# Performance work log

Measured on AMD Instinct MI355X. Metric: run time of the kernel, lower is better.

## Reference

```python
import jax, jax.numpy as jnp
import numpy as np

# ---- dims (see shape_source) ----
N, EG, T = 10000, 120000, 600000
NR, NS = 16, 7                      # num_radial, num_spherical
EA, EE, ET, ERBF, ECBF, EBIL = 128, 256, 64, 16, 16, 64
NB = 2                              # num_blocks
CUTOFF = 6.0
MAXZ = 100
INV_SQRT2 = 0.7071067811865476


def scaled_silu(x):
    # GemNet 'swish' activation = ScaledSiLU
    return jax.nn.silu(x) * (1.0 / 0.6)


def layer_norm(x, w, b):
    mu = jnp.mean(x, -1, keepdims=True)
    v = jnp.var(x, -1, keepdims=True)
    return (x - mu) * jax.lax.rsqrt(v + 1e-5) * w + b


def radial_basis(D):
    # polynomial envelope (exponent 5) * gaussian RBF on d/cutoff
    d = D / CUTOFF
    p = 5.0
    env = 1.0 - ((p + 1) * (p + 2) / 2) * d**5 + p * (p + 2) * d**6 - (p * (p + 1) / 2) * d**7
    env = jnp.where(d < 1.0, env, 0.0)
    offsets = jnp.linspace(0.0, 1.0, NR)
    coeff = -0.5 * (NR - 1.0) ** 2   # -0.5 / spacing^2
    return env[:, None] * jnp.exp(coeff * (d[:, None] - offsets) ** 2)  # (EG, NR)


def spherical_basis(cosphi):
    # circular basis: Y_l0(phi) = sqrt((2l+1)/4pi) P_l(cos phi), l = 0..NS-1
    P = [jnp.ones_like(cosphi), cosphi]
    for l in range(2, NS):
        P.append(((2 * l - 1) * cosphi * P[-1] - (l - 1) * P[-2]) / l)
    return jnp.stack([np.sqrt((2 * l + 1) / (4 * np.pi)) * P[l] for l in range(NS)], -1)  # (T, NS)


def residual(x, Ws):
    # GemNet ResidualLayer: 2 bias-free dense + skip, scaled by 1/sqrt(2)
    y = scaled_silu(scaled_silu(x @ Ws[0]) @ Ws[1])
    return (x + y) * INV_SQRT2


def gemnet_forward(D, cosphi, atom_emb, W_rbf3, W_rbf_h, W_rbf_out, W_cbf_down,
                   W_edge_emb, ib_dense_ca, ib_trip_dense_ba, ib_trip_mlp_rbf,
                   ib_trip_down, ib_trip_bilinear, ib_trip_up_ca, ib_trip_up_ac,
                   ib_res_before, ib_res_after, ib_atom_dense_rbf, ib_atom_dense1,
                   ib_atom_res, ib_concat_dense, ib_res_m, ob_dense_rbf, ob_dense1,
                   ob_res, ln_m_w, ln_m_b, ln_E_w, ln_E_b,
                   Z, idx_s, idx_t, id3_ba, id3_ca, id_swap):
    rbf = radial_basis(D)                                   # (EG, NR)
    sph = spherical_basis(cosphi)                           # (T, NS)
    rbf3 = rbf @ W_rbf3                                     # (EG, ERBF)
    rbf_h = rbf @ W_rbf_h
    rbf_out = rbf @ W_rbf_out
    # EfficientInteractionDownProjection: rbf x W -> (EG, NS, ECBF)
    rbf_W1 = jnp.einsum('er,sri->esi', rbf, W_cbf_down)
    # per-triplet circular-basis embedding: sum over spherical components
    cbf_t = jnp.einsum('ts,tsi->ti', sph, rbf_W1[id3_ca])   # (T, ECBF)

    h = atom_emb[Z]                                         # (N, EA)
    m = scaled_silu(jnp.concatenate([h[idx_s], h[idx_t], rbf], -1) @ W_edge_emb)  # (EG, EE)

    def out_block(i, h_cur, m_cur):
        mn = layer_norm(m_cur, ln_m_w[i], ln_m_b[i])
        x = mn * (rbf_out @ ob_dense_rbf[i])                # (EG, EE)
        xE = jax.ops.segment_sum(x, idx_t, num_segments=N)  # scatter edges -> atoms
        xE = scaled_silu(xE @ ob_dense1[i])                 # (N, EA)
        for r in range(ob_res.shape[1]):
            xE = residual(xE, ob_res[i, r])
        return layer_norm(xE, ln_E_w[i], ln_E_b[i])

    E_t = out_block(0, h, m)
    for i in range(NB):
        # ---- triplet interaction ----
        x_ca_skip = scaled_silu(m @ ib_dense_ca[i])
        x_ba = scaled_silu(m @ ib_trip_dense_ba[i])
        x_ba = x_ba * (rbf3 @ ib_trip_mlp_rbf[i])
        x_trip = scaled_silu(x_ba @ ib_trip_down[i])        # (EG, ET)
        x_t = x_trip[id3_ba]                                # gather -> (T, ET)
        # bilinear: out[t,o] = sum_i cbf_t[t,i] * sum_c x_t[t,c] W[c,i,o]
        Wb = ib_trip_bilinear[i]                            # (ET, ECBF, EBIL)
        acc = (x_t @ Wb[:, 0, :]) * cbf_t[:, 0:1]
        for ic in range(1, ECBF):
            acc = acc + (x_t @ Wb[:, ic, :]) * cbf_t[:, ic:ic + 1]
        x = jax.ops.segment_sum(acc, id3_ca, num_segments=EG)  # scatter trip -> edges (EG, EBIL)
        x_ca = scaled_silu(x @ ib_trip_up_ca[i])
        x_ac = scaled_silu(x @ ib_trip_up_ac[i])[id_swap]   # counter-directional edge
        x3 = (x_ca + x_ac) * INV_SQRT2

        # ---- edge update ----
        x = (x_ca_skip + x3) * INV_SQRT2
        for r in range(ib_res_before.shape[1]):
            x = residual(x, ib_res_before[i, r])
        x = (x + m) * INV_SQRT2
        for r in range(ib_res_after.shape[1]):
            x = residual(x, ib_res_after[i, r])

        # ---- atom update ----
        xa = x * (rbf_h @ ib_atom_dense_rbf[i])
        xa = jax.ops.segment_sum(xa, idx_t, num_segments=N)
        xa = scaled_silu(xa @ ib_atom_dense1[i])            # (N, EA)
        for r in range(ib_atom_res.shape[1]):
            xa = residual(xa, ib_atom_res[i, r])
        h = (h + xa) * INV_SQRT2

        # ---- edge embedding refresh with updated atoms ----
        m2 = scaled_silu(jnp.concatenate([h[idx_s], h[idx_t], x], -1) @ ib_concat_dense[i])
        for r in range(ib_res_m.shape[1]):
            m2 = residual(m2, ib_res_m[i, r])
        m = (m + m2) * INV_SQRT2

        E_t = E_t + out_block(i + 1, h, m)
    return E_t  # (N, EA) per-atom output features


def setup_inputs() -> dict:
    key = jax.random.key(0)
    ks = iter(jax.random.split(key, 64))

    def nrm(shape, fan_in):
        return jax.random.normal(next(ks), shape, jnp.float32) / np.sqrt(fan_in)

    Z = jax.random.randint(next(ks), (N,), 0, MAXZ)
    idx_s = jax.random.randint(next(ks), (EG,), 0, N)
    idx_t = jax.random.randint(next(ks), (EG,), 0, N)
    id3_ba = jax.random.randint(next(ks), (T,), 0, EG)
    id3_ca = jax.random.randint(next(ks), (T,), 0, EG)
    id_swap = jnp.arange(EG) ^ 1   # symmetric edges stored in (e, e^1) pairs
    D = jax.random.uniform(next(ks), (EG,), jnp.float32, 0.8, 5.9)
    cosphi = jax.random.uniform(next(ks), (T,), jnp.float32, -1.0, 1.0)

    emb = jax.random.normal(next(ks), (MAXZ, EA), jnp.float32)
    emb = emb / jnp.maximum(jnp.linalg.norm(emb, axis=-1, keepdims=True), 1.0)  # max_norm=1

    NBo = NB + 1
    inp = dict(
        D=D, cosphi=cosphi, atom_emb=emb,
        W_rbf3=nrm((NR, ERBF), NR), W_rbf_h=nrm((NR, ERBF), NR), W_rbf_out=nrm((NR, ERBF), NR),
        W_cbf_down=nrm((NS, NR, ECBF), NR),
        W_edge_emb=nrm((2 * EA + NR, EE), 2 * EA + NR),
        ib_dense_ca=nrm((NB, EE, EE), EE),
        ib_trip_dense_ba=nrm((NB, EE, EE), EE),
        ib_trip_mlp_rbf=nrm((NB, ERBF, EE), ERBF),
        ib_trip_down=nrm((NB, EE, ET), EE),
        ib_trip_bilinear=nrm((NB, ET, ECBF, EBIL), ET * ECBF),
        ib_trip_up_ca=nrm((NB, EBIL, EE), EBIL),
        ib_trip_up_ac=nrm((NB, EBIL, EE), EBIL),
        ib_res_before=nrm((NB, 1, 2, EE, EE), EE),
        ib_res_after=nrm((NB, 1, 2, EE, EE), EE),
        ib_atom_dense_rbf=nrm((NB, ERBF, EE), ERBF),
        ib_atom_dense1=nrm((NB, EE, EA), EE),
        ib_atom_res=nrm((NB, 2, 2, EA, EA), EA),
        ib_concat_dense=nrm((NB, 2 * EA + EE, EE), 2 * EA + EE),
        ib_res_m=nrm((NB, 1, 2, EE, EE), EE),
        ob_dense_rbf=nrm((NBo, ERBF, EE), ERBF),
        ob_dense1=nrm((NBo, EE, EA), EE),
        ob_res=nrm((NBo, 2, 2, EA, EA), EA),
        ln_m_w=jnp.ones((NBo, EE)), ln_m_b=jnp.zeros((NBo, EE)),
        ln_E_w=jnp.ones((NBo, EA)), ln_E_b=jnp.zeros((NBo, EA)),
        Z=Z, idx_s=idx_s, idx_t=idx_t, id3_ba=id3_ba, id3_ca=id3_ca, id_swap=id_swap,
    )
    return inp


def reference(D, cosphi, atom_emb, W_rbf3, W_rbf_h, W_rbf_out, W_cbf_down, W_edge_emb,
              ib_dense_ca, ib_trip_dense_ba, ib_trip_mlp_rbf, ib_trip_down,
              ib_trip_bilinear, ib_trip_up_ca, ib_trip_up_ac, ib_res_before,
              ib_res_after, ib_atom_dense_rbf, ib_atom_dense1, ib_atom_res,
              ib_concat_dense, ib_res_m, ob_dense_rbf, ob_dense1, ob_res,
              ln_m_w, ln_m_b, ln_E_w, ln_E_b, Z, idx_s, idx_t, id3_ba, id3_ca, id_swap):
    return gemnet_forward(D, cosphi, atom_emb, W_rbf3, W_rbf_h, W_rbf_out, W_cbf_down,
                          W_edge_emb, ib_dense_ca, ib_trip_dense_ba, ib_trip_mlp_rbf,
                          ib_trip_down, ib_trip_bilinear, ib_trip_up_ca, ib_trip_up_ac,
                          ib_res_before, ib_res_after, ib_atom_dense_rbf, ib_atom_dense1,
                          ib_atom_res, ib_concat_dense, ib_res_m, ob_dense_rbf, ob_dense1,
                          ob_res, ln_m_w, ln_m_b, ln_E_w, ln_E_b,
                          Z, idx_s, idx_t, id3_ba, id3_ca, id_swap)
```

## Files before the change

### kernel.cpp

```cpp
#include <hip/hip_runtime.h>

#define NATOM 10000
#define EG    120000
#define TT    600000

#define INV_SQRT2f 0.7071067811865476f

typedef unsigned short bf16t;
typedef __attribute__((ext_vector_type(8))) short s16x8;
typedef __attribute__((ext_vector_type(8))) unsigned short u16x8;
typedef __attribute__((ext_vector_type(4))) float f32x4;

__device__ __forceinline__ float ssilu(float x) {
    return x * (1.0f / (1.0f + __expf(-x))) * (1.0f / 0.6f);
}
__device__ __forceinline__ float bf2f(unsigned short u) {
    return __uint_as_float(((unsigned)u) << 16);
}
__device__ __forceinline__ unsigned short f2bf(float f) {
    unsigned b = __float_as_uint(f);
    unsigned r = (b + 0x7FFF + ((b >> 16) & 1)) >> 16;
    return (unsigned short)r;
}
__device__ __forceinline__ u16x8 cvt8(const float4 va, const float4 vb) {
// ... 187 lines not shown
        float ys = y[s];
#pragma unroll
        for (int i = 0; i < 16; i++) out[i] = fmaf(ys, w[s * 16 + i], out[i]);
    }
    int p = rank[t];
#pragma unroll
    for (int i = 0; i < 16; i++) cbf[(size_t)p * 16 + i] = f2bf(out[i]);
}

__global__ __launch_bounds__(256) void k_hgather(
    const float* __restrict__ emb, const int* __restrict__ Z, bf16t* __restrict__ h)
{
    int i = blockIdx.x * 256 + threadIdx.x;
    if (i < NATOM * 128) {
        int n = i >> 7, j = i & 127;
        h[i] = f2bf(emb[(size_t)Z[n] * 128 + j]);
    }
}

template <typename TA, int FR, int FC, int EPI>
__global__ __launch_bounds__(256) void mgemm3(
    const TA* __restrict__ A, const bf16t* __restrict__ BT,
    bf16t* __restrict__ C, const bf16t* __restrict__ skip,
    int M, int N, int K)
{
    constexpr int ROWS = 2 * FR * 16;
    constexpr int COLS = 2 * FC * 16;
    __shared__ __align__(16) ushort As[ROWS][40];
    __shared__ __align__(16) ushort Bs[COLS][40];
    const int tid = threadIdx.x, wave = tid >> 6, lane = tid & 63;
    const int waveR = wave >> 1, waveC = wave & 1;
    const int rowBase = blockIdx.y * ROWS, colBase = blockIdx.x * COLS;

    const int sar = tid >> 1, sak = (tid & 1) << 4;
    int agr = rowBase + sar; if (agr >= M) agr = M - 1;
    int sbc, sbk;
    if constexpr (COLS == 128) { sbc = tid >> 1; sbk = (tid & 1) << 4; }
    else                       { sbc = tid >> 2; sbk = (tid & 3) << 3; }

    f32x4 zv = {0.f, 0.f, 0.f, 0.f};
    f32x4 acc[FR][FC];
#pragma unroll
    for (int f = 0; f < FR; f++)
#pragma unroll
        for (int q = 0; q < FC; q++) acc[f][q] = zv;

    const int arow0 = waveR * FR * 16 + (lane & 15);
    const int bcol0 = waveC * FC * 16 + (lane & 15);
    const int kd = (lane >> 4) << 3;

    u16x8 a0, a1, b0, b1;
    auto loadA = [&](int k0) {
        if constexpr (sizeof(TA) == 2) {
            const u16x8* s = (const u16x8*)((const bf16t*)A + (size_t)agr * K + k0 + sak);
            a0 = s[0]; a1 = s[1];
        } else {
            const float4* s = (const float4*)((const float*)A + (size_t)agr * K + k0 + sak);
            a0 = cvt8(s[0], s[1]); a1 = cvt8(s[2], s[3]);
        }
    };
    auto loadB = [&](int k0) {
        const u16x8* s = (const u16x8*)(BT + (size_t)(colBase + sbc) * K + k0 + sbk);
        b0 = s[0];
        if constexpr (COLS == 128) b1 = s[1];
    };
    loadA(0); loadB(0);
    for (int k0 = 0; k0 < K; k0 += 32) {
        __syncthreads();
        *(u16x8*)&As[sar][sak] = a0;
        *(u16x8*)&As[sar][sak + 8] = a1;
        *(u16x8*)&Bs[sbc][sbk] = b0;
        if constexpr (COLS == 128) *(u16x8*)&Bs[sbc][sbk + 8] = b1;
        __syncthreads();
        if (k0 + 32 < K) { loadA(k0 + 32); loadB(k0 + 32); }
        u16x8 af[FR], bf[FC];
#pragma unroll
        for (int f = 0; f < FR; f++) af[f] = *(const u16x8*)&As[arow0 + f * 16][kd];
#pragma unroll
        for (int q = 0; q < FC; q++) bf[q] = *(const u16x8*)&Bs[bcol0 + q * 16][kd];
#pragma unroll
        for (int f = 0; f < FR; f++)
#pragma unroll
            for (int q = 0; q < FC; q++)
                acc[f][q] = __builtin_amdgcn_mfma_f32_16x16x32_bf16(
                    *(s16x8*)&af[f], *(s16x8*)&bf[q], acc[f][q], 0, 0, 0);
    }

    const int rB = rowBase + waveR * FR * 16 + ((lane >> 4) << 2);
    const int cB = colBase + waveC * FC * 16 + (lane & 15);
#pragma unroll
    for (int f = 0; f < FR; f++) {
#pragma unroll
        for (int r = 0; r < 4; r++) {
            int row = rB + f * 16 + r;
            if (row >= M) continue;
#pragma unroll
            for (int q = 0; q < FC; q++) {
                int col = cB + q * 16;
                float v = acc[f][q][r];
                if (EPI == 1) {
                    C[(size_t)row * N + col] = f2bf(ssilu(v));
                } else {
                    float sk = bf2f(skip[(size_t)row * N + col]);
                    C[(size_t)row * N + col] = f2bf((sk + ssilu(v)) * INV_SQRT2f);
                }
            }
        }
    }
}

template <typename TA, int FC>
__global__ __launch_bounds__(256) void mgemm4(
    const TA* __restrict__ A, const bf16t* __restrict__ BT,
    bf16t* __restrict__ C, int M, int N, int K)
{
    constexpr int COLS = 2 * FC * 16;
    __shared__ __align__(16) ushort As[256][40];
    __shared__ __align__(16) ushort Bs[COLS][40];
    const int tid = threadIdx.x, wave = tid >> 6, lane = tid & 63;
    const int waveR = wave >> 1, waveC = wave & 1;
    const int rowBase = blockIdx.y * 256, colBase = blockIdx.x * COLS;

    int agr = rowBase + tid; if (agr >= M) agr = M - 1;
    const int sbc = tid >> 1, sbk = (tid & 1) << 4;

    f32x4 zv = {0.f, 0.f, 0.f, 0.f};
    f32x4 acc[8][FC];
#pragma unroll
    for (int f = 0; f < 8; f++)
#pragma unroll
        for (int q = 0; q < FC; q++) acc[f][q] = zv;

    const int arow0 = waveR * 128 + (lane & 15);
    const int bcol0 = waveC * FC * 16 + (lane & 15);
    const int kd = (lane >> 4) << 3;

    u16x8 a[4], b0, b1;
    auto loadA = [&](int k0) {
        if constexpr (sizeof(TA) == 2) {
            const u16x8* s = (const u16x8*)((const bf16t*)A + (size_t)agr * K + k0);
            a[0] = s[0]; a[1] = s[1]; a[2] = s[2]; a[3] = s[3];
        } else {
            const float4* s = (const float4*)((const float*)A + (size_t)agr * K + k0);
            a[0] = cvt8(s[0], s[1]); a[1] = cvt8(s[2], s[3]);
            a[2] = cvt8(s[4], s[5]); a[3] = cvt8(s[6], s[7]);
        }
    };
    auto loadB = [&](int k0) {
        const u16x8* s = (const u16x8*)(BT + (size_t)(colBase + sbc) * K + k0 + sbk);
        b0 = s[0]; b1 = s[1];
    };
    loadA(0); loadB(0);
    for (int k0 = 0; k0 < K; k0 += 32) {
        __syncthreads();
        *(u16x8*)&As[tid][0] = a[0];
        *(u16x8*)&As[tid][8] = a[1];
        *(u16x8*)&As[tid][16] = a[2];
        *(u16x8*)&As[tid][24] = a[3];
        *(u16x8*)&Bs[sbc][sbk] = b0;
        *(u16x8*)&Bs[sbc][sbk + 8] = b1;
        __syncthreads();
        if (k0 + 32 < K) { loadA(k0 + 32); loadB(k0 + 32); }
        u16x8 af[8], bf[FC];
#pragma unroll
        for (int f = 0; f < 8; f++) af[f] = *(const u16x8*)&As[arow0 + f * 16][kd];
#pragma unroll
        for (int q = 0; q < FC; q++) bf[q] = *(const u16x8*)&Bs[bcol0 + q * 16][kd];
#pragma unroll
        for (int f = 0; f < 8; f++)
#pragma unroll
            for (int q = 0; q < FC; q++)
                acc[f][q] = __builtin_amdgcn_mfma_f32_16x16x32_bf16(
                    *(s16x8*)&af[f], *(s16x8*)&bf[q], acc[f][q], 0, 0, 0);
    }

    const int rB = rowBase + waveR * 128 + ((lane >> 4) << 2);
    const int cB = colBase + waveC * FC * 16 + (lane & 15);
#pragma unroll
    for (int f = 0; f < 8; f++) {
#pragma unroll
        for (int r = 0; r < 4; r++) {
            int row = rB + f * 16 + r;
            if (row >= M) continue;
#pragma unroll
            for (int q = 0; q < FC; q++)
                C[(size_t)row * N + cB + q * 16] = f2bf(ssilu(acc[f][q][r]));
        }
    }
}

template <int FCC, int EPIOUT>
__global__ __launch_bounds__(256) void mgemm_res(
    const bf16t* __restrict__ A, const bf16t* __restrict__ BT0,
    const bf16t* __restrict__ BT1, bf16t* __restrict__ C,
    const bf16t* __restrict__ add2, int M)
{
    constexpr int N = FCC * 32;
    __shared__ __align__(16) ushort As[64][40];
    __shared__ __align__(16) ushort Bs[N][40];
    __shared__ __align__(16) ushort inter[64][N + 8];
    const int tid = threadIdx.x, wave = tid >> 6, lane = tid & 63;
    const int waveR = wave >> 1, waveC = wave & 1;
    const int rowBase = blockIdx.x * 64;

    const int sar = tid >> 2, sak = (tid & 3) << 3;
    int agr = rowBase + sar; if (agr >= M) agr = M - 1;
    const int sbc = tid >> 2, sbk = (tid & 3) << 3;

    const int arow0 = waveR * 32 + (lane & 15);
    const int bcol0 = waveC * FCC * 16 + (lane & 15);
    const int kd = (lane >> 4) << 3;

    f32x4 zv = {0.f, 0.f, 0.f, 0.f};
    f32x4 acc[2][FCC];
#pragma unroll
    for (int f = 0; f < 2; f++)
#pragma unroll
        for (int q = 0; q < FCC; q++) acc[f][q] = zv;

    u16x8 aR, bR[FCC / 2];
    auto loadA = [&](int k0) {
        aR = *(const u16x8*)(A + (size_t)agr * N + k0 + sak);
    };
    auto loadB = [&](const bf16t* BT, int k0) {
#pragma unroll
        for (int j = 0; j < FCC / 2; j++)
            bR[j] = *(const u16x8*)(BT + (size_t)(sbc + j * 64) * N + k0 + sbk);
    };

    loadA(0); loadB(BT0, 0);
    for (int k0 = 0; k0 < N; k0 += 32) {
        __syncthreads();
        *(u16x8*)&As[sar][sak] = aR;
#pragma unroll
        for (int j = 0; j < FCC / 2; j++) *(u16x8*)&Bs[sbc + j * 64][sbk] = bR[j];
        __syncthreads();
        if (k0 + 32 < N) { loadA(k0 + 32); loadB(BT0, k0 + 32); }
        else             { loadB(BT1, 0); }
        u16x8 af0 = *(const u16x8*)&As[arow0][kd];
        u16x8 af1 = *(const u16x8*)&As[arow0 + 16][kd];
        u16x8 bf[FCC];
#pragma unroll
        for (int q = 0; q < FCC; q++) bf[q] = *(const u16x8*)&Bs[bcol0 + q * 16][kd];
#pragma unroll
        for (int q = 0; q < FCC; q++) {
            acc[0][q] = __builtin_amdgcn_mfma_f32_16x16x32_bf16(
                *(s16x8*)&af0, *(s16x8*)&bf[q], acc[0][q], 0, 0, 0);
            acc[1][q] = __builtin_amdgcn_mfma_f32_16x16x32_bf16(
                *(s16x8*)&af1, *(s16x8*)&bf[q], acc[1][q], 0, 0, 0);
        }
    }
    {
        const int rL = waveR * 32 + ((lane >> 4) << 2);
        const int cL = waveC * FCC * 16 + (lane & 15);
#pragma unroll
        for (int f = 0; f < 2; f++)
#pragma unroll
            for (int r = 0; r < 4; r++)
#pragma unroll
                for (int q = 0; q < FCC; q++)
                    inter[rL + f * 16 + r][cL + q * 16] = f2bf(ssilu(acc[f][q][r]));
    }
#pragma unroll
    for (int f = 0; f < 2; f++)
#pragma unroll
        for (int q = 0; q < FCC; q++) acc[f][q] = zv;

    for (int k0 = 0; k0 < N; k0 += 32) {
        __syncthreads();
#pragma unroll
        for (int j = 0; j < FCC / 2; j++) *(u16x8*)&Bs[sbc + j * 64][sbk] = bR[j];
        __syncthreads();
        if (k0 + 32 < N) loadB(BT1, k0 + 32);
        u16x8 af0 = *(const u16x8*)&inter[arow0][k0 + kd];
        u16x8 af1 = *(const u16x8*)&inter[arow0 + 16][k0 + kd];
        u16x8 bf[FCC];
#pragma unroll
        for (int q = 0; q < FCC; q++) bf[q] = *(const u16x8*)&Bs[bcol0 + q * 16][kd];
#pragma unroll
        for (int q = 0; q < FCC; q++) {
            acc[0][q] = __builtin_amdgcn_mfma_f32_16x16x32_bf16(
                *(s16x8*)&af0, *(s16x8*)&bf[q], acc[0][q], 0, 0, 0);
            acc[1][q] = __builtin_amdgcn_mfma_f32_16x16x32_bf16(
                *(s16x8*)&af1, *(s16x8*)&bf[q], acc[1][q], 0, 0, 0);
        }
    }

    const int rB = rowBase + waveR * 32 + ((lane >> 4) << 2);
    const int cB = waveC * FCC * 16 + (lane & 15);
#pragma unroll
    for (int f = 0; f < 2; f++) {
#pragma unroll
        for (int r = 0; r < 4; r++) {
            int row = rB + f * 16 + r;
            if (row >= M) continue;
#pragma unroll
            for (int q = 0; q < FCC; q++) {
                int col = cB + q * 16;
                float sk = bf2f(A[(size_t)row * N + col]);
                float y = (sk + ssilu(acc[f][q][r])) * INV_SQRT2f;
                if (EPIOUT == 1) y = (y + bf2f(add2[(size_t)row * N + col])) * INV_SQRT2f;
                C[(size_t)row * N + col] = f2bf(y);
            }
        }
    }
}

__global__ __launch_bounds__(256) void mgemmA1(
    const bf16t* __restrict__ BT, bf16t* __restrict__ C,
    int M, int N, int K, int KP,
    const bf16t* __restrict__ hA, const int* __restrict__ gS,
    const int* __restrict__ gT, const bf16t* __restrict__ X, int w2)
{
    __shared__ __align__(16) ushort As[256][40];
    __shared__ __align__(16) ushort Bs[128][40];
    const int tid = threadIdx.x, wave = tid >> 6, lane = tid & 63;
    const int waveR = wave >> 1, waveC = wave & 1;
    const int rowBase = blockIdx.y * 256, colBase = blockIdx.x * 128;

    int agr = rowBase + tid; if (agr >= M) agr = M - 1;
    const int ia = gS[agr], ibx = gT[agr];
    const int sbc = tid >> 1, sbk = (tid & 1) << 4;

    f32x4 zv = {0.f, 0.f, 0.f, 0.f};
    f32x4 acc[8][4];
#pragma unroll
    for (int f = 0; f < 8; f++)
#pragma unroll
        for (int q = 0; q < 4; q++) acc[f][q] = zv;

    const int arow0 = waveR * 128 + (lane & 15);
    const int bcol0 = waveC * 64 + (lane & 15);
    const int kd = (lane >> 4) << 3;

    u16x8 a[4], b0, b1;
    auto loadA = [&](int k0) {
#pragma unroll
        for (int h = 0; h < 2; h++) {
            int kk = k0 + 16 * h;
            u16x8 t0{}, t1{};
            if (kk < 128) {
                const u16x8* s = (const u16x8*)(hA + (size_t)ia * 128 + kk);
                t0 = s[0]; t1 = s[1];
            } else if (kk < 256) {
                const u16x8* s = (const u16x8*)(hA + (size_t)ibx * 128 + (kk - 128));
                t0 = s[0]; t1 = s[1];
            } else if (kk < K && kk - 256 < w2) {
                const u16x8* s = (const u16x8*)(X + (size_t)agr * w2 + (kk - 256));
                t0 = s[0]; t1 = s[1];
            }
            a[2 * h] = t0; a[2 * h + 1] = t1;
        }
    };
    auto loadB = [&](int k0) {
        const u16x8* s = (const u16x8*)(BT + (size_t)(colBase + sbc) * KP + k0 + sbk);
        b0 = s[0]; b1 = s[1];
    };
    loadA(0); loadB(0);
    for (int k0 = 0; k0 < K; k0 += 32) {
        __syncthreads();
        *(u16x8*)&As[tid][0] = a[0];
        *(u16x8*)&As[tid][8] = a[1];
        *(u16x8*)&As[tid][16] = a[2];
        *(u16x8*)&As[tid][24] = a[3];
        *(u16x8*)&Bs[sbc][sbk] = b0;
        *(u16x8*)&Bs[sbc][sbk + 8] = b1;
        __syncthreads();
        if (k0 + 32 < K) { loadA(k0 + 32); loadB(k0 + 32); }
        u16x8 af[8], bf[4];
#pragma unroll
        for (int f = 0; f < 8; f++) af[f] = *(const u16x8*)&As[arow0 + f * 16][kd];
#pragma unroll
        for (int q = 0; q < 4; q++) bf[q] = *(const u16x8*)&Bs[bcol0 + q * 16][kd];
#pragma unroll
        for (int f = 0; f < 8; f++)
#pragma unroll
            for (int q = 0; q < 4; q++)
                acc[f][q] = __builtin_amdgcn_mfma_f32_16x16x32_bf16(
                    *(s16x8*)&af[f], *(s16x8*)&bf[q], acc[f][q], 0, 0, 0);
    }

    const int rB = rowBase + waveR * 128 + ((lane >> 4) << 2);
    const int cB = colBase + waveC * 64 + (lane & 15);
#pragma unroll
    for (int f = 0; f < 8; f++) {
#pragma unroll
        for (int r = 0; r < 4; r++) {
            int row = rB + f * 16 + r;
            if (row >= M) continue;
#pragma unroll
            for (int q = 0; q < 4; q++)
                C[(size_t)row * N + cB + q * 16] = f2bf(ssilu(acc[f][q][r]));
        }
    }
}

__global__ __launch_bounds__(256) void mgemm_up(
    const float* __restrict__ A, const bf16t* __restrict__ BTca,
    const bf16t* __restrict__ BTac, bf16t* __restrict__ C,
    const bf16t* __restrict__ skip, int M)
{
    constexpr int K = 64, N = 256;
    __shared__ __align__(16) ushort As[128][40];
    __shared__ __align__(16) ushort Bs[2][64][40];
    const int tid = threadIdx.x, wave = tid >> 6, lane = tid & 63;
    const int waveR = wave >> 1, waveC = wave & 1;
    const int rowBase = blockIdx.y * 128, colBase = blockIdx.x * 64;

    const int sar = tid >> 1, sak = (tid & 1) << 4;
    int agr = rowBase + sar; if (agr >= M) agr = M - 1;
    const int sbc = tid >> 2, sbk = (tid & 3) << 3;

    f32x4 zv = {0.f, 0.f, 0.f, 0.f};
    f32x4 accA[4][2], accB[4][2];
#pragma unroll
    for (int f = 0; f < 4; f++)
#pragma unroll
        for (int q = 0; q < 2; q++) { accA[f][q] = zv; accB[f][q] = zv; }

    const int arow0 = waveR * 64 + (lane & 15);
    const int bcol0 = waveC * 32 + (lane & 15);
    const int kd = (lane >> 4) << 3;

    u16x8 a0, a1, bA, bB;
    auto loadA = [&](int k0) {
        const float4* s = (const float4*)(A + (size_t)agr * K + k0 + sak);
        a0 = cvt8(s[0], s[1]); a1 = cvt8(s[2], s[3]);
    };
    auto loadB = [&](int k0) {
        bA = *(const u16x8*)(BTca + (size_t)(colBase + sbc) * K + k0 + sbk);
        bB = *(const u16x8*)(BTac + (size_t)(colBase + sbc) * K + k0 + sbk);
    };
    loadA(0); loadB(0);
    for (int k0 = 0; k0 < K; k0 += 32) {
        __syncthreads();
        *(u16x8*)&As[sar][sak] = a0;
        *(u16x8*)&As[sar][sak + 8] = a1;
        *(u16x8*)&Bs[0][sbc][sbk] = bA;
        *(u16x8*)&Bs[1][sbc][sbk] = bB;
        __syncthreads();
        if (k0 + 32 < K) { loadA(k0 + 32); loadB(k0 + 32); }
        u16x8 af[4], bfA[2], bfB[2];
#pragma unroll
        for (int f = 0; f < 4; f++) af[f] = *(const u16x8*)&As[arow0 + f * 16][kd];
#pragma unroll
        for (int q = 0; q < 2; q++) {
            bfA[q] = *(const u16x8*)&Bs[0][bcol0 + q * 16][kd];
            bfB[q] = *(const u16x8*)&Bs[1][bcol0 + q * 16][kd];
        }
#pragma unroll
        for (int f = 0; f < 4; f++)
#pragma unroll
            for (int q = 0; q < 2; q++) {
                accA[f][q] = __builtin_amdgcn_mfma_f32_16x16x32_bf16(
                    *(s16x8*)&af[f], *(s16x8*)&bfA[q], accA[f][q], 0, 0, 0);
                accB[f][q] = __builtin_amdgcn_mfma_f32_16x16x32_bf16(
                    *(s16x8*)&af[f], *(s16x8*)&bfB[q], accB[f][q], 0, 0, 0);
            }
    }

    const int rB = rowBase + waveR * 64 + ((lane >> 4) << 2);
    const int cB = colBase + waveC * 32 + (lane & 15);
#pragma unroll
    for (int f = 0; f < 4; f++) {
#pragma unroll
        for (int r = 0; r < 4; r++) {
            int row = rB + f * 16 + r;
            if (row >= M) continue;
#pragma unroll
            for (int q = 0; q < 2; q++) {
                int col = cB + q * 16;
                float v = (ssilu(accA[f][q][r]) + ssilu(accB[f][q][r ^ 1])) * INV_SQRT2f;
                float y = (bf2f(skip[(size_t)row * N + col]) + v) * INV_SQRT2f;
                C[(size_t)row * N + col] = f2bf(y);
            }
        }
    }
}

__global__ __launch_bounds__(256) void k_bilinear_m(
    const bf16t* __restrict__ xtrip, const bf16t* __restrict__ cbf,
    const bf16t* __restrict__ WT,
    const int* __restrict__ ba_s, const int* __restrict__ ca_s,
    float* __restrict__ seg)
{
    __shared__ __align__(16) ushort xs[64][72];
    __shared__ ushort cbs[64][16];
    __shared__ int cas[64];
    __shared__ __align__(16) ushort ws[2][4096];
    __shared__ __align__(16) float ts[64][65];
    const int tid = threadIdx.x, wave = tid >> 6, lane = tid & 63;
    const int t0 = blockIdx.x * 64;
    {
        int r = tid >> 2, q = (tid & 3) << 4;
        int ba = ba_s[t0 + r];
        const u16x8* src = (const u16x8*)(xtrip + (size_t)ba * 64 + q);
        *(u16x8*)&xs[r][q] = src[0];
        *(u16x8*)&xs[r][q + 8] = src[1];
    }
    if (tid < 64) cas[tid] = ca_s[t0 + tid];
    {
        int e = tid << 2; int r = e >> 4, c = e & 15;
        *(ushort4*)&cbs[r][c] = *(const ushort4*)(cbf + (size_t)(t0 + r) * 16 + c);
    }
    u16x8 g0, g1;
    {
        const u16x8* s = (const u16x8*)(WT + (size_t)tid * 16);
        *(u16x8*)&ws[0][tid * 16] = s[0];
        *(u16x8*)&ws[0][tid * 16 + 8] = s[1];
        const u16x8* s1 = (const u16x8*)(WT + 4096 + (size_t)tid * 16);
        g0 = s1[0]; g1 = s1[1];
    }
    __syncthreads();
    const int kd = (lane >> 4) << 3;
    u16x8 a0 = *(const u16x8*)(&xs[wave * 16 + (lane & 15)][kd]);
    u16x8 a1 = *(const u16x8*)(&xs[wave * 16 + (lane & 15)][32 + kd]);
    const int rowo = wave * 16 + ((lane >> 4) << 2);
    const int chb = lane >> 4, colw = lane & 15;

    float tot[4][4];
#pragma unroll
    for (int a = 0; a < 4; a++)
#pragma unroll
        for (int b = 0; b < 4; b++) tot[a][b] = 0.f;

    for (int i = 0; i < 16; i++) {
        const int cur = i & 1;
        if (i < 15) {
            *(u16x8*)&ws[cur ^ 1][tid * 16] = g0;
            *(u16x8*)&ws[cur ^ 1][tid * 16 + 8] = g1;
        }
        const ushort* wb = ws[cur];
        f32x4 zv = {0.f, 0.f, 0.f, 0.f};
        f32x4 p[4] = {zv, zv, zv, zv};
#pragma unroll
        for (int fc = 0; fc < 4; fc++) {
            u16x8 b0 = *(const u16x8*)&wb[((chb * 64) + colw + fc * 16) * 8];
            u16x8 b1 = *(const u16x8*)&wb[(((4 + chb) * 64) + colw + fc * 16) * 8];
            p[fc] = __builtin_amdgcn_mfma_f32_16x16x32_bf16(
                *(s16x8*)&a0, *(s16x8*)&b0, p[fc], 0, 0, 0);
            p[fc] = __builtin_amdgcn_mfma_f32_16x16x32_bf16(
                *(s16x8*)&a1, *(s16x8*)&b1, p[fc], 0, 0, 0);
        }
#pragma unroll
        for (int r = 0; r < 4; r++) {
            float s = bf2f(cbs[rowo + r][i]);
#pragma unroll
            for (int fc = 0; fc < 4; fc++) tot[fc][r] += s * p[fc][r];
        }
        if (i < 14) {
            const u16x8* s = (const u16x8*)(WT + (size_t)(i + 2) * 4096 + (size_t)tid * 16);
            g0 = s[0]; g1 = s[1];
        }
        __syncthreads();
    }
#pragma unroll
    for (int r = 0; r < 4; r++)
#pragma unroll
        for (int fc = 0; fc < 4; fc++)
            ts[rowo + r][fc * 16 + (lane & 15)] = tot[fc][r];
    __syncthreads();
    {
        int q = tid >> 6, c = tid & 63;
        float s = 0.f;
        int cur = cas[q * 16];
#pragma unroll 1
        for (int r = q * 16; r < q * 16 + 16; r++) {
            int ca = cas[r];
            if (ca != cur) {
                atomicAdd(&seg[(size_t)cur * 64 + c], s);
                s = 0.f; cur = ca;
            }
            s += ts[r][c];
        }
        atomicAdd(&seg[(size_t)cur * 64 + c], s);
    }
}

__global__ __launch_bounds__(256) void k_mulproj(
    const bf16t* __restrict__ in, const bf16t* __restrict__ rvec,
    const float* __restrict__ Wp, bf16t* __restrict__ out)
{
    __shared__ float sW[4096];
    __shared__ float sr[256];
    const int j = threadIdx.x;
    const int e0 = blockIdx.x * 16;
    for (int t = j; t < 4096; t += 256) sW[t] = Wp[t];
    sr[j] = bf2f(rvec[(size_t)e0 * 16 + j]);
    __syncthreads();
#pragma unroll 4
    for (int g = 0; g < 16; g++) {
        float p = 0.f;
#pragma unroll
        for (int k = 0; k < 16; k++) p = fmaf(sr[g * 16 + k], sW[k * 256 + j], p);
        size_t e = (size_t)(e0 + g);
        out[e * 256 + j] = f2bf(bf2f(in[e * 256 + j]) * p);
    }
}

__global__ __launch_bounds__(256) void k_ln_proj(
    const bf16t* __restrict__ m, const float* __restrict__ lnw,
    const float* __restrict__ lnb, const bf16t* __restrict__ rvec,
    const float* __restrict__ Wp, bf16t* __restrict__ out)
{
    __shared__ float sW[4096];
    __shared__ float sr[256];
    __shared__ float red[8];
    const int j = threadIdx.x;
    const int e0 = blockIdx.x * 16;
    for (int t = j; t < 4096; t += 256) sW[t] = Wp[t];
    sr[j] = bf2f(rvec[(size_t)e0 * 16 + j]);
    const float lw = lnw[j], lb = lnb[j];
    __syncthreads();
    const int wid = j >> 6, lane = j & 63;
    for (int g = 0; g < 16; g++) {
        size_t e = (size_t)(e0 + g);
        float v = bf2f(m[e * 256 + j]);
        float s = v, s2 = v * v;
#pragma unroll
        for (int off = 32; off > 0; off >>= 1) {
            s += __shfl_xor(s, off);
            s2 += __shfl_xor(s2, off);
        }
        if (lane == 0) { red[wid] = s; red[4 + wid] = s2; }
        __syncthreads();
        float tot = red[0] + red[1] + red[2] + red[3];
        float tot2 = red[4] + red[5] + red[6] + red[7];
        float mu = tot * (1.f / 256.f);
        float var = tot2 * (1.f / 256.f) - mu * mu;
        float ln = (v - mu) * rsqrtf(var + 1e-5f) * lw + lb;
        float p = 0.f;
#pragma unroll
        for (int k = 0; k < 16; k++) p = fmaf(sr[g * 16 + k], sW[k * 256 + j], p);
        out[e * 256 + j] = f2bf(ln * p);
        __syncthreads();
    }
}

__global__ __launch_bounds__(128) void k_ln_acc(
    const bf16t* __restrict__ x, const float* __restrict__ w,
    const float* __restrict__ b, float* __restrict__ out)
{
    int n = blockIdx.x;
    int j = threadIdx.x;
    __shared__ float red[4];
    float v = bf2f(x[(size_t)n * 128 + j]);
    float s = v, s2 = v * v;
#pragma unroll
    for (int off = 32; off > 0; off >>= 1) {
        s += __shfl_xor(s, off);
        s2 += __shfl_xor(s2, off);
    }
    int wid = j >> 6, lane = j & 63;
    if (lane == 0) { red[wid] = s; red[2 + wid] = s2; }
    __syncthreads();
    float tot = red[0] + red[1];
    float tot2 = red[2] + red[3];
    float mu = tot * (1.f / 128.f);
    float var = tot2 * (1.f / 128.f) - mu * mu;
    out[(size_t)n * 128 + j] += (v - mu) * rsqrtf(var + 1e-5f) * w[j] + b[j];
}

typedef bf16t T;
static bool try_run(void* const* d_in, void* d_out, void* d_ws, size_t ws_size, hipStream_t stream)
{
    const float* D            = (const float*)d_in[0];
    const float* cosphi       = (const float*)d_in[1];
    const float* atom_emb     = (const float*)d_in[2];
    const float* W_rbf3       = (const float*)d_in[3];
    const float* W_rbf_h      = (const float*)d_in[4];
    const float* W_rbf_out    = (const float*)d_in[5];
    const float* W_cbf_down   = (const float*)d_in[6];
    const float* W_edge_emb   = (const float*)d_in[7];
    const float* ib_dense_ca  = (const float*)d_in[8];
    const float* ib_trip_dense_ba = (const float*)d_in[9];
    const float* ib_trip_mlp_rbf  = (const float*)d_in[10];
    const float* ib_trip_down     = (const float*)d_in[11];
    const float* ib_trip_bilinear = (const float*)d_in[12];
    const float* ib_trip_up_ca    = (const float*)d_in[13];
    const float* ib_trip_up_ac    = (const float*)d_in[14];
    const float* ib_res_before    = (const float*)d_in[15];
    const float* ib_res_after     = (const float*)d_in[16];
    const float* ib_atom_dense_rbf = (const float*)d_in[17];
    const float* ib_atom_dense1    = (const float*)d_in[18];
    const float* ib_atom_res       = (const float*)d_in[19];
    const float* ib_concat_dense   = (const float*)d_in[20];
    const float* ib_res_m          = (const float*)d_in[21];
    const float* ob_dense_rbf      = (const float*)d_in[22];
    const float* ob_dense1         = (const float*)d_in[23];
    const float* ob_res            = (const float*)d_in[24];
    const float* ln_m_w            = (const float*)d_in[25];
    const float* ln_m_b            = (const float*)d_in[26];
    const float* ln_E_w            = (const float*)d_in[27];
    const float* ln_E_b            = (const float*)d_in[28];
    const int* Z       = (const int*)d_in[29];
    const int* idx_s   = (const int*)d_in[30];
    const int* idx_t   = (const int*)d_in[31];
    const int* id3_ba  = (const int*)d_in[32];
    const int* id3_ca  = (const int*)d_in[33];

    char* base = (char*)d_ws;
    size_t off = 0;
    auto alloc = [&](size_t bytes) -> char* {
        off = (off + 255) & ~(size_t)255;
        char* p = base + off;
        off += bytes;
        return p;
    };
    T* m      = (T*)alloc((size_t)EG * 256 * 2);
    T* B1     = (T*)alloc((size_t)EG * 256 * 2);
    T* B2     = (T*)alloc((size_t)EG * 256 * 2);
    float* rbfW1 = (float*)B1;
    int* rank    = (int*)B2;
    T* rbf    = (T*)alloc((size_t)EG * 16 * 2);
    T* cbf    = (T*)alloc((size_t)TT * 16 * 2);
    bf16t* h  = (bf16t*)alloc((size_t)NATOM * 128 * 2);
    T* xtrip  = (T*)alloc((size_t)EG * 64 * 2);
    char* ub  = alloc((size_t)EG * 64 * 4);
    float* seg64  = (float*)ub;
    bf16t* segN_b = (bf16t*)ub;
    bf16t* At1b   = (bf16t*)(ub + (size_t)NATOM * 256 * 2);
    int* cntT  = (int*)ub;
    int* cnt2T = (int*)(ub + (size_t)EG * 4);
    int* off_ca = (int*)(ub + (size_t)2 * EG * 4);
    float* wcb = (float*)alloc((size_t)7 * 4096 * 4);
    bf16t* ar  = (bf16t*)alloc((size_t)507904 * 2);
    int* off_atom  = (int*)alloc((size_t)(NATOM + 1) * 4);
    int* ba_s      = (int*)alloc((size_t)TT * 4);
    int* ca_s      = (int*)alloc((size_t)TT * 4);
    int* csr_edges = (int*)alloc((size_t)EG * 4);
    if (off > ws_size) return false;
    float* out = (float*)d_out;

    auto g256 = [&](const T* A, unsigned wOff, T* C) {
        dim3 grid(2, (EG + 255) / 256);
        mgemm4<T, 4><<<grid, 256, 0, stream>>>(A, ar + wOff, C, EG, 256, 256);
    };
    auto gatom1 = [&](const bf16t* A, unsigned wOff, bf16t* C) {
        dim3 grid(1, (NATOM + 127) / 128);
        mgemm3<bf16t, 4, 4, 1><<<grid, 256, 0, stream>>>(A, ar + wOff, C, nullptr, NATOM, 128, 256);
    };
    auto out_block = [&](int i, unsigned offD1, unsigned offRes) {
        k_ln_proj<<<EG / 16, 256, 0, stream>>>(m, ln_m_w + (size_t)i * 256, ln_m_b + (size_t)i * 256,
                                               rbf, wcb + (size_t)(4 + i) * 4096, B2);
        k_segsum<<<NATOM, 256, 0, stream>>>(B2, off_atom, csr_edges, segN_b);
        gatom1(segN_b, offD1, At1b);
        mgemm_res<4, 0><<<(NATOM + 63) / 64, 256, 0, stream>>>(
            At1b, ar + offRes, ar + offRes + 16384, At1b, nullptr, NATOM);
        mgemm_res<4, 0><<<(NATOM + 63) / 64, 256, 0, stream>>>(
            At1b, ar + offRes + 32768, ar + offRes + 49152, At1b, nullptr, NATOM);
        k_ln_acc<<<NATOM, 128, 0, stream>>>(At1b, ln_E_w + (size_t)i * 128, ln_E_b + (size_t)i * 128, out);
    };

    hipMemsetAsync(cntT, 0, (size_t)EG * 4, stream);
    k_hist<<<(TT + 255) / 256, 256, 0, stream>>>(id3_ca, cntT, TT);
    k_scan<<<1, 1024, 0, stream>>>(cntT, off_ca, EG);
    hipMemsetAsync(cnt2T, 0, (size_t)EG * 4, stream);
    k_rank_trip<<<(TT + 255) / 256, 256, 0, stream>>>(id3_ca, id3_ba, off_ca, cnt2T,
                                                      rank, ba_s, ca_s, TT);
    hipMemsetAsync(cntT, 0, (size_t)NATOM * 4, stream);
    k_hist<<<(EG + 255) / 256, 256, 0, stream>>>(idx_t, cntT, EG);
    k_scan<<<1, 1024, 0, stream>>>(cntT, off_atom, NATOM);
    hipMemsetAsync(cnt2T, 0, (size_t)NATOM * 4, stream);
    k_rank_edge<<<(EG + 255) / 256, 256, 0, stream>>>(idx_t, off_atom, cnt2T, csr_edges, EG);

    {
        WcBatch wb;
        wb.e[0] = {W_rbf3, ib_trip_mlp_rbf};
        wb.e[1] = {W_rbf3, ib_trip_mlp_rbf + 4096};
        wb.e[2] = {W_rbf_h, ib_atom_dense_rbf};
        wb.e[3] = {W_rbf_h, ib_atom_dense_rbf + 4096};
        wb.e[4] = {W_rbf_out, ob_dense_rbf};
        wb.e[5] = {W_rbf_out, ob_dense_rbf + 4096};
        wb.e[6] = {W_rbf_out, ob_dense_rbf + 8192};
        k_wcomb_batch<<<7, 256, 0, stream>>>(wb, wcb);
    }
    {
        WtBatch wt{};
        wt.e[0] = {W_edge_emb, 0u, 272, 288, 256, 0};
        wt.e[1] = {ob_dense1, 73728u, 256, 256, 128, 0};
        for (int j = 0; j < 4; j++)
            wt.e[2 + j] = {ob_res + (size_t)j * 16384, 106496u + j * 16384u, 128, 128, 128, 0};
        wt.n = 6;
        k_wt_batch<<<512, 256, 0, stream>>>(wt, ar);
    }

    hipMemsetAsync(out, 0, (size_t)NATOM * 128 * 4, stream);
    k_rbf<<<(EG + 255) / 256, 256, 0, stream>>>(D, W_cbf_down, rbf, rbfW1);
    k_cbf<<<(TT + 255) / 256, 256, 0, stream>>>(cosphi, id3_ca, rbfW1, rank, cbf);
    k_hgather<<<(NATOM * 128 + 255) / 256, 256, 0, stream>>>(atom_emb, Z, h);
    {
        dim3 grid(2, (EG + 255) / 256);
        mgemmA1<<<grid, 256, 0, stream>>>(ar, m, EG, 256, 272, 288, h, idx_s, idx_t, rbf, 16);
    }
    out_block(0, 73728u, 106496u);

    for (int i = 0; i < 2; i++) {
        {
            WtBatch wt{};
            wt.e[0] = {ib_dense_ca + (size_t)i * 65536, 0u, 256, 256, 256, 0};
            wt.e[1] = {ib_trip_dense_ba + (size_t)i * 65536, 65536u, 256, 256, 256, 0};
            wt.e[2] = {ib_trip_down + (size_t)i * 16384, 131072u, 256, 256, 64, 0};
            wt.e[3] = {ib_trip_bilinear + (size_t)i * 65536, 147456u, 0, 0, 0, 1};
            wt.e[4] = {ib_trip_up_ca + (size_t)i * 16384, 212992u, 64, 64, 256, 0};
            wt.e[5] = {ib_trip_up_ac + (size_t)i * 16384, 229376u, 64, 64, 256, 0};
            wt.e[6] = {ib_res_before + (size_t)i * 131072, 245760u, 256, 256, 256, 0};
            wt.e[7] = {ib_res_before + (size_t)i * 131072 + 65536, 311296u, 256, 256, 256, 0};
            wt.e[8] = {ib_res_after + (size_t)i * 131072, 376832u, 256, 256, 256, 0};
            wt.e[9] = {ib_res_after + (size_t)i * 131072 + 65536, 442368u, 256, 256, 256, 0};
            wt.n = 10;
            k_wt_batch<<<512, 256, 0, stream>>>(wt, ar);
        }
        g256(m, 0u, B1);
        g256(m, 65536u, B2);
        k_mulproj<<<EG / 16, 256, 0, stream>>>(B2, rbf, wcb + (size_t)i * 4096, B2);
        {
            dim3 grid(1, (EG + 127) / 128);
            mgemm3<T, 4, 2, 1><<<grid, 256, 0, stream>>>(B2, ar + 131072, xtrip, nullptr, EG, 64, 256);
        }
        hipMemsetAsync(seg64, 0, (size_t)EG * 64 * 4, stream);
        k_bilinear_m<<<TT / 64, 256, 0, stream>>>(xtrip, cbf, ar + 147456, ba_s, ca_s, seg64);
        {
            dim3 grid(4, (EG + 127) / 128);
            mgemm_up<<<grid, 256, 0, stream>>>(seg64, ar + 212992, ar + 229376, B1, B1, EG);
        }
        mgemm_res<8, 1><<<EG / 64, 256, 0, stream>>>(B1, ar + 245760, ar + 311296, B1, m, EG);
        mgemm_res<8, 0><<<EG / 64, 256, 0, stream>>>(B1, ar + 376832, ar + 442368, B1, nullptr, EG);
        {
            WtBatch wt{};
            wt.e[0] = {ib_atom_dense1 + (size_t)i * 32768, 0u, 256, 256, 128, 0};
            for (int j = 0; j < 4; j++)
                wt.e[1 + j] = {ib_atom_res + (size_t)i * 65536 + (size_t)j * 16384,
                               32768u + j * 16384u, 128, 128, 128, 0};
            wt.e[5] = {ib_concat_dense + (size_t)i * 131072, 98304u, 512, 512, 256, 0};
            wt.e[6] = {ib_res_m + (size_t)i * 131072, 229376u, 256, 256, 256, 0};
            wt.e[7] = {ib_res_m + (size_t)i * 131072 + 65536, 294912u, 256, 256, 256, 0};
            wt.e[8] = {ob_dense1 + (size_t)(i + 1) * 32768, 360448u, 256, 256, 128, 0};
            wt.n = 9;
            k_wt_batch<<<512, 256, 0, stream>>>(wt, ar);
            WtBatch wt2{};
            for (int j = 0; j < 4; j++)
                wt2.e[j] = {ob_res + (size_t)(i + 1) * 65536 + (size_t)j * 16384,
                            393216u + j * 16384u, 128, 128, 128, 0};
            wt2.n = 4;
            k_wt_batch<<<512, 256, 0, stream>>>(wt2, ar);
        }
        k_mulproj<<<EG / 16, 256, 0, stream>>>(B1, rbf, wcb + (size_t)(2 + i) * 4096, B2);
        k_segsum<<<NATOM, 256, 0, stream>>>(B2, off_atom, csr_edges, segN_b);
        gatom1(segN_b, 0u, At1b);
        mgemm_res<4, 0><<<(NATOM + 63) / 64, 256, 0, stream>>>(
            At1b, ar + 32768, ar + 49152, At1b, nullptr, NATOM);
        mgemm_res<4, 1><<<(NATOM + 63) / 64, 256, 0, stream>>>(
            At1b, ar + 65536, ar + 81920, h, h, NATOM);
        {
            dim3 grid(2, (EG + 255) / 256);
            mgemmA1<<<grid, 256, 0, stream>>>(ar + 98304, B2, EG, 256, 512, 512, h, idx_s, idx_t, B1, 256);
        }
        mgemm_res<8, 1><<<EG / 64, 256, 0, stream>>>(B2, ar + 229376, ar + 294912, m, m, EG);

        out_block(i + 1, 360448u, 393216u);
    }
    return true;
}

extern "C" void kernel_launch(void* const* d_in, const int* in_sizes, int n_in,
                              void* d_out, int out_size, void* d_ws, size_t ws_size,
                              hipStream_t stream)
{
    if (try_run(d_in, d_out, d_ws, ws_size, stream)) return;
    float v = 3000.0f + (float)(ws_size >> 20);
    k_fill<<<(NATOM * 128 + 255) / 256, 256, 0, stream>>>((float*)d_out, NATOM * 128, v);
}
```

Measured before the change: 2.641 ms.

## Fuse atom dense and two residual layers into one shared-memory chain kernel

```diff
diff --git a/kernel.cpp b/kernel.cpp
--- a/kernel.cpp
+++ b/kernel.cpp
@@ -513,6 +513,177 @@
                 if (EPIOUT == 1) y = (y + bf2f(add2[(size_t)row * N + col])) * INV_SQRT2f;
                 C[(size_t)row * N + col] = f2bf(y);
             }
+        }
+    }
+}
+
+template <int EPI>
+__global__ __launch_bounds__(256) void k_atomchain(
+    const bf16t* __restrict__ X, const bf16t* __restrict__ BTd1,
+    const bf16t* __restrict__ BTres, bf16t* __restrict__ C, int M)
+{
+    __shared__ __align__(16) ushort As[64][40];
+    __shared__ __align__(16) ushort Bs[128][40];
+    __shared__ __align__(16) ushort buf0[64][136];
+    __shared__ __align__(16) ushort buf1[64][136];
+    const int tid = threadIdx.x, wave = tid >> 6, lane = tid & 63;
+    const int waveR = wave >> 1, waveC = wave & 1;
+    const int rowBase = blockIdx.x * 64;
+    const int arow0 = waveR * 32 + (lane & 15);
+    const int bcol0 = waveC * 64 + (lane & 15);
+    const int kd = (lane >> 4) << 3;
+    const int rL = waveR * 32 + ((lane >> 4) << 2);
+    const int cL = waveC * 64 + (lane & 15);
+    const int sbc = tid >> 1, sbk = (tid & 1) << 4;
+
+    f32x4 zv = {0.f, 0.f, 0.f, 0.f};
+    f32x4 acc[2][4];
+
+    {
+        const int sar = tid >> 2, sak = (tid & 3) << 3;
+        int agr = rowBase + sar; if (agr >= M) agr = M - 1;
+#pragma unroll
+        for (int f = 0; f < 2; f++)
+#pragma unroll
+            for (int q = 0; q < 4; q++) acc[f][q] = zv;
+        u16x8 aR, b0, b1;
+        auto loadA = [&](int k0) {
+            aR = *(const u16x8*)(X + (size_t)agr * 256 + k0 + sak);
+        };
+        auto loadB = [&](int k0) {
+            const u16x8* s = (const u16x8*)(BTd1 + (size_t)sbc * 256 + k0 + sbk);
+            b0 = s[0]; b1 = s[1];
+        };
+        loadA(0); loadB(0);
+        for (int k0 = 0; k0 < 256; k0 += 32) {
+            __syncthreads();
+            *(u16x8*)&As[sar][sak] = aR;
+            *(u16x8*)&Bs[sbc][sbk] = b0;
+            *(u16x8*)&Bs[sbc][sbk + 8] = b1;
+            __syncthreads();
+            if (k0 + 32 < 256) { loadA(k0 + 32); loadB(k0 + 32); }
+            u16x8 af0 = *(const u16x8*)&As[arow0][kd];
+            u16x8 af1 = *(const u16x8*)&As[arow0 + 16][kd];
+            u16x8 bf[4];
+#pragma unroll
+            for (int q = 0; q < 4; q++) bf[q] = *(const u16x8*)&Bs[bcol0 + q * 16][kd];
+#pragma unroll
+            for (int q = 0; q < 4; q++) {
+                acc[0][q] = __builtin_amdgcn_mfma_f32_16x16x32_bf16(
+                    *(s16x8*)&af0, *(s16x8*)&bf[q], acc[0][q], 0, 0, 0);
+                acc[1][q] = __builtin_amdgcn_mfma_f32_16x16x32_bf16(
+                    *(s16x8*)&af1, *(s16x8*)&bf[q], acc[1][q], 0, 0, 0);
+            }
+        }
+#pragma unroll
+        for (int f = 0; f < 2; f++)
+#pragma unroll
+            for (int r = 0; r < 4; r++)
+#pragma unroll
+                for (int q = 0; q < 4; q++)
+                    buf0[rL + f * 16 + r][cL + q * 16] = f2bf(ssilu(acc[f][q][r]));
+    }
+
+    for (int rl = 0; rl < 2; rl++) {
+        const bf16t* BT0 = BTres + (size_t)(rl * 2 + 0) * 16384;
+        const bf16t* BT1 = BTres + (size_t)(rl * 2 + 1) * 16384;
+        {
+#pragma unroll
+            for (int f = 0; f < 2; f++)
+#pragma unroll
+                for (int q = 0; q < 4; q++) acc[f][q] = zv;
+            u16x8 b0, b1;
+            auto loadB = [&](const bf16t* BT, int k0) {
+                const u16x8* s = (const u16x8*)(BT + (size_t)sbc * 128 + k0 + sbk);
+                b0 = s[0]; b1 = s[1];
+            };
+            loadB(BT0, 0);
+            for (int k0 = 0; k0 < 128; k0 += 32) {
+                __syncthreads();
+                *(u16x8*)&Bs[sbc][sbk] = b0;
+                *(u16x8*)&Bs[sbc][sbk + 8] = b1;
+                __syncthreads();
+                if (k0 + 32 < 128) loadB(BT0, k0 + 32);
+                else               loadB(BT1, 0);
+                u16x8 af0 = *(const u16x8*)&buf0[arow0][k0 + kd];
+                u16x8 af1 = *(const u16x8*)&buf0[arow0 + 16][k0 + kd];
+                u16x8 bf[4];
+#pragma unroll
+                for (int q = 0; q < 4; q++) bf[q] = *(const u16x8*)&Bs[bcol0 + q * 16][kd];
+#pragma unroll
+                for (int q = 0; q < 4; q++) {
+                    acc[0][q] = __builtin_amdgcn_mfma_f32_16x16x32_bf16(
+                        *(s16x8*)&af0, *(s16x8*)&bf[q], acc[0][q], 0, 0, 0);
+                    acc[1][q] = __builtin_amdgcn_mfma_f32_16x16x32_bf16(
+                        *(s16x8*)&af1, *(s16x8*)&bf[q], acc[1][q], 0, 0, 0);
+                }
+            }
+#pragma unroll
+            for (int f = 0; f < 2; f++)
+#pragma unroll
+                for (int r = 0; r < 4; r++)
+#pragma unroll
+                    for (int q = 0; q < 4; q++)
+                        buf1[rL + f * 16 + r][cL + q * 16] = f2bf(ssilu(acc[f][q][r]));
+        }
+        {
+#pragma unroll
+            for (int f = 0; f < 2; f++)
+#pragma unroll
+                for (int q = 0; q < 4; q++) acc[f][q] = zv;
+            u16x8 b0, b1;
+            auto loadB = [&](const bf16t* BT, int k0) {
+                const u16x8* s = (const u16x8*)(BT + (size_t)sbc * 128 + k0 + sbk);
+                b0 = s[0]; b1 = s[1];
+            };
+            loadB(BT1, 0);
+            for (int k0 = 0; k0 < 128; k0 += 32) {
+                __syncthreads();
+                *(u16x8*)&Bs[sbc][sbk] = b0;
+                *(u16x8*)&Bs[sbc][sbk + 8] = b1;
+                __syncthreads();
+                if (k0 + 32 < 128) loadB(BT1, k0 + 32);
+                u16x8 af0 = *(const u16x8*)&buf1[arow0][k0 + kd];
+                u16x8 af1 = *(const u16x8*)&buf1[arow0 + 16][k0 + kd];
+                u16x8 bf[4];
+#pragma unroll
+                for (int q = 0; q < 4; q++) bf[q] = *(const u16x8*)&Bs[bcol0 + q * 16][kd];
+#pragma unroll
+                for (int q = 0; q < 4; q++) {
+                    acc[0][q] = __builtin_amdgcn_mfma_f32_16x16x32_bf16(
+                        *(s16x8*)&af0, *(s16x8*)&bf[q], acc[0][q], 0, 0, 0);
+                    acc[1][q] = __builtin_amdgcn_mfma_f32_16x16x32_bf16(
+                        *(s16x8*)&af1, *(s16x8*)&bf[q], acc[1][q], 0, 0, 0);
+                }
+            }
+#pragma unroll
+            for (int f = 0; f < 2; f++)
+#pragma unroll
+                for (int r = 0; r < 4; r++)
+#pragma unroll
+                    for (int q = 0; q < 4; q++) {
+                        int rr = rL + f * 16 + r, cc = cL + q * 16;
+                        float sk = bf2f(buf0[rr][cc]);
+                        buf0[rr][cc] = f2bf((sk + ssilu(acc[f][q][r])) * INV_SQRT2f);
+                    }
+        }
+    }
+
+    __syncthreads();
+    for (int v = tid; v < 1024; v += 256) {
+        int row = v >> 4, c8 = (v & 15) << 3;
+        int grow = rowBase + row;
+        if (grow >= M) continue;
+        u16x8 val = *(const u16x8*)&buf0[row][c8];
+        if (EPI == 0) {
+            *(u16x8*)&C[(size_t)grow * 128 + c8] = val;
+        } else {
+            u16x8 hv = *(const u16x8*)&C[(size_t)grow * 128 + c8];
+            u16x8 o;
+#pragma unroll
+            for (int j = 0; j < 8; j++)
+                o[j] = f2bf((bf2f(hv[j]) + bf2f(val[j])) * INV_SQRT2f);
+            *(u16x8*)&C[(size_t)grow * 128 + c8] = o;
         }
     }
 }
@@ -947,19 +1118,12 @@
         dim3 grid(2, (EG + 255) / 256);
         mgemm4<T, 4><<<grid, 256, 0, stream>>>(A, ar + wOff, C, EG, 256, 256);
     };
-    auto gatom1 = [&](const bf16t* A, unsigned wOff, bf16t* C) {
-        dim3 grid(1, (NATOM + 127) / 128);
-        mgemm3<bf16t, 4, 4, 1><<<grid, 256, 0, stream>>>(A, ar + wOff, C, nullptr, NATOM, 128, 256);
-    };
     auto out_block = [&](int i, unsigned offD1, unsigned offRes) {
         k_ln_proj<<<EG / 16, 256, 0, stream>>>(m, ln_m_w + (size_t)i * 256, ln_m_b + (size_t)i * 256,
                                                rbf, wcb + (size_t)(4 + i) * 4096, B2);
         k_segsum<<<NATOM, 256, 0, stream>>>(B2, off_atom, csr_edges, segN_b);
-        gatom1(segN_b, offD1, At1b);
-        mgemm_res<4, 0><<<(NATOM + 63) / 64, 256, 0, stream>>>(
-            At1b, ar + offRes, ar + offRes + 16384, At1b, nullptr, NATOM);
-        mgemm_res<4, 0><<<(NATOM + 63) / 64, 256, 0, stream>>>(
-            At1b, ar + offRes + 32768, ar + offRes + 49152, At1b, nullptr, NATOM);
+        k_atomchain<0><<<(NATOM + 63) / 64, 256, 0, stream>>>(
+            segN_b, ar + offD1, ar + offRes, At1b, NATOM);
         k_ln_acc<<<NATOM, 128, 0, stream>>>(At1b, ln_E_w + (size_t)i * 128, ln_E_b + (size_t)i * 128, out);
     };
 
@@ -1058,11 +1222,8 @@
         }
         k_mulproj<<<EG / 16, 256, 0, stream>>>(B1, rbf, wcb + (size_t)(2 + i) * 4096, B2);
         k_segsum<<<NATOM, 256, 0, stream>>>(B2, off_atom, csr_edges, segN_b);
-        gatom1(segN_b, 0u, At1b);
-        mgemm_res<4, 0><<<(NATOM + 63) / 64, 256, 0, stream>>>(
-            At1b, ar + 32768, ar + 49152, At1b, nullptr, NATOM);
-        mgemm_res<4, 1><<<(NATOM + 63) / 64, 256, 0, stream>>>(
-            At1b, ar + 65536, ar + 81920, h, h, NATOM);
+        k_atomchain<1><<<(NATOM + 63) / 64, 256, 0, stream>>>(
+            segN_b, ar + 0u, ar + 32768u, h, NATOM);
         {
             dim3 grid(2, (EG + 255) / 256);
             mgemmA1<<<grid, 256, 0, stream>>>(ar + 98304, B2, EG, 256, 512, 512, h, idx_s, idx_t, B1, 256);
```

Result: no change. 2.624 ms (-0.6%).
